# Kernel optimization log

Hardware: AMD Instinct MI355X
Metric: run time of the kernel (lower is better)

Reference implementation:

```python
import jax, jax.numpy as jnp
import numpy as np

B, N, D, RNN, K_TOPK = 32, 2000, 128, 640, 64


def setup_inputs() -> dict:
    key = jax.random.key(0)
    ks = jax.random.split(key, 16)
    s = 1.0 / np.sqrt(D)
    return {
        "Ahat": jax.random.uniform(ks[0], (B, N, N), dtype=jnp.float32),
        "node_embs": jax.random.normal(ks[1], (B, N, D), dtype=jnp.float32),
        "ht": jax.random.normal(ks[2], (B, RNN), dtype=jnp.float32),
        "prev_D": jax.random.normal(ks[3], (B, D, D), dtype=jnp.float32) * s,
        "mapper_w": jax.random.normal(ks[4], (D, RNN), dtype=jnp.float32) / np.sqrt(RNN),
        "mapper_b": jnp.zeros((D,), jnp.float32),
        "Wu": jax.random.normal(ks[5], (D, D), jnp.float32) * s,
        "Uu": jax.random.normal(ks[6], (D, D), jnp.float32) * s,
        "bu": jnp.zeros((D, D), jnp.float32),
        "Wr": jax.random.normal(ks[7], (D, D), jnp.float32) * s,
        "Ur": jax.random.normal(ks[8], (D, D), jnp.float32) * s,
        "br": jnp.zeros((D, D), jnp.float32),
        "Wh": jax.random.normal(ks[9], (D, D), jnp.float32) * s,
        "Uh": jax.random.normal(ks[10], (D, D), jnp.float32) * s,
        "bh": jnp.zeros((D, D), jnp.float32),
        "static_w": jax.random.normal(ks[11], (D, D), jnp.float32) * s,
    }


def _gate(W, U, b, x, h, act):
    # W,U: [D,D]; x,h: [B,D,D]; bias broadcasts over batch
    return act(jnp.einsum('ij,bjk->bik', W, x) + jnp.einsum('ij,bjk->bik', U, h) + b)


def reference(Ahat, node_embs, ht, prev_D, mapper_w, mapper_b,
              Wu, Uu, bu, Wr, Ur, br, Wh, Uh, bh, static_w):
    act = jax.nn.relu
    # ---- TopK_with_h ----
    scorer = jnp.tanh(jax.lax.stop_gradient(ht) @ mapper_w.T + mapper_b)     # [B,D]
    scores = jnp.einsum('bnd,bd->bn', node_embs, scorer)                      # [B,N]
    scores = scores / jnp.linalg.norm(scorer, axis=1, keepdims=True)
    _, topk_idx = jax.lax.top_k(scores, K_TOPK)                               # [B,K_TOPK]
    rep = D // K_TOPK + 1
    idx = jnp.tile(topk_idx, (1, rep))[:, :D]                                 # [B,D] selected node ids
    sel = jnp.take_along_axis(node_embs, idx[:, :, None], axis=1)             # [B,D,Dfeat]
    sel = sel * jnp.tanh(jnp.take_along_axis(scores, idx, axis=1))[..., None]
    logp = jax.nn.log_softmax(scores, axis=1)
    p = jnp.exp(logp)
    entropy = -(p * logp).sum(axis=1)                                         # [B]
    policy_score = jnp.take_along_axis(logp, idx, axis=1).mean(axis=1)        # [B]
    x = sel.transpose(0, 2, 1)                                                # [B,Dfeat,D]
    # ---- mat_GRU_cell: evolve GCN weights ----
    update = _gate(Wu, Uu, bu, x, prev_D, jax.nn.sigmoid)
    reset = _gate(Wr, Ur, br, x, prev_D, jax.nn.sigmoid)
    htilda = _gate(Wh, Uh, bh, x, reset * prev_D, jnp.tanh)
    Dw = (1.0 - update) * prev_D + update * htilda                            # [B,D,D]
    # ---- gather selected subgraph ----
    ne = jnp.take_along_axis(node_embs, idx[:, :, None], axis=1)              # [B,D,Dfeat]
    A = jnp.take_along_axis(Ahat, idx[:, :, None], axis=1)                    # [B,D,N]
    A = jnp.take_along_axis(A, idx[:, None, :], axis=2)                       # [B,D,D]
    di = A.sum(axis=1) ** -0.5                                                # [B,D]
    A = di[:, None, :] * A * jax.lax.stop_gradient(di[:, :, None])
    # ---- GCN with evolved + static weights ----
    h1 = act(jnp.einsum('bkj,bjd->bkd', A, jnp.einsum('bjd,bde->bje', ne, Dw)))
    h2 = act(jnp.einsum('bkj,bjd->bkd', A, jnp.einsum('bjd,de->bje', h1, static_w)))
    out = (h1 + h2) * 0.5                                                     # [B,D,Dfeat]
    return (out, policy_score, scorer, entropy)
```

## Files before the change

### kernel.cpp

```cpp
#include <hip/hip_runtime.h>
#include <math.h>


namespace {
constexpr int B_ = 32;
constexpr int N_ = 2000;
constexpr int D_ = 128;
constexpr int R_ = 640;

constexpr size_t OFF_SCORER = 0;
constexpr size_t OFF_INVN   = 4096;
constexpr size_t OFF_CANDV  = 4128;
constexpr size_t OFF_CANDI  = 20512;
constexpr size_t OFF_STATS  = 36896;
constexpr size_t OFF_TKI    = 37664;
constexpr size_t OFF_T0     = 39712;
constexpr size_t OFF_NE0T   = 41760;
constexpr size_t OFF_A0R    = 303904;
constexpr size_t OFF_DW     = 434976;
constexpr size_t OFF_H1     = 959264;

__global__ __launch_bounds__(1024) void k1_scorer(
    const float* __restrict__ ht, const float* __restrict__ mw,
    const float* __restrict__ mb, float* __restrict__ scorer,
    float* __restrict__ invn, float* __restrict__ outScorer) {
  const int b = blockIdx.x, t = threadIdx.x;
  const int d = t & 127, slice = t >> 7;
  __shared__ float sh[R_];
  __shared__ float part[8][128];
  __shared__ float red[2];
  for (int j = t; j < R_; j += 1024) sh[j] = ht[b * R_ + j];
  __syncthreads();
  const float* wp = mw + (size_t)d * R_ + slice * 80;
  const float* hh = sh + slice * 80;
  float acc = 0.f;
  #pragma unroll
  for (int j = 0; j < 80; j += 4) {
    float4 wv = *reinterpret_cast<const float4*>(wp + j);
    acc += wv.x * hh[j] + wv.y * hh[j + 1] + wv.z * hh[j + 2] + wv.w * hh[j + 3];
  }
  part[slice][d] = acc;
  __syncthreads();
  if (t < 128) {
    float a = mb[t];
    #pragma unroll
    for (int s = 0; s < 8; ++s) a += part[s][t];
    const float sv = tanhf(a);
    scorer[b * D_ + t] = sv;
    outScorer[b * D_ + t] = sv;
    float ss = sv * sv;
    #pragma unroll
    for (int o = 32; o > 0; o >>= 1) ss += __shfl_down(ss, o);
    if ((t & 63) == 0) red[t >> 6] = ss;
  }
  __syncthreads();
  if (t == 0) invn[b] = 1.0f / sqrtf(red[0] + red[1]);
}

__global__ __launch_bounds__(512) void k2_scores(
    const float* __restrict__ node, const float* __restrict__ scorer,
    const float* __restrict__ invn, float* __restrict__ cand_v,
    int* __restrict__ cand_i, float* __restrict__ stats) {
  const int b = blockIdx.x, c = blockIdx.y, t = threadIdx.x;
  const int cand = t & 255, s = t >> 8;
  const int lane = t & 63, w = t >> 6;
  __shared__ float sc[D_];
  __shared__ float pd[256][2];
  __shared__ float cv[256];
  __shared__ int ci[256];
  __shared__ int pr[256][2];
  __shared__ float r1[8], r2[8];
  if (t < D_) sc[t] = scorer[b * D_ + t];
  __syncthreads();
  const float inv = invn[b];
  const int n = c * 250 + cand;
  const bool valid = cand < 250;
  {
    float acc = 0.f;
    if (valid) {
      const float* row = node + ((size_t)b * N_ + n) * D_ + s * 64;
      const float* scp = sc + s * 64;
      #pragma unroll
      for (int j = 0; j < 64; j += 4) {
        float4 a = *reinterpret_cast<const float4*>(row + j);
        acc += a.x * scp[j] + a.y * scp[j + 1] + a.z * scp[j + 2] + a.w * scp[j + 3];
      }
    }
    pd[cand][s] = acc;
  }
  __syncthreads();
  float v = -INFINITY;
  if (s == 0 && valid) v = (pd[cand][0] + pd[cand][1]) * inv;
  float m = v;
  #pragma unroll
  for (int o = 32; o > 0; o >>= 1) m = fmaxf(m, __shfl_xor(m, o));
  if (lane == 0) r1[w] = m;
  __syncthreads();
  float Mc = r1[0];
  #pragma unroll
  for (int q = 1; q < 8; ++q) Mc = fmaxf(Mc, r1[q]);
  __syncthreads();
  float se = 0.f, sx = 0.f;
  if (s == 0 && valid) {
    const float x = v - Mc;
    const float e = expf(x);
    se = e;
    sx = x * e;
  }
  #pragma unroll
  for (int o = 32; o > 0; o >>= 1) {
    se += __shfl_xor(se, o);
    sx += __shfl_xor(sx, o);
  }
  if (lane == 0) { r1[w] = se; r2[w] = sx; }
  if (s == 0) {
    cv[cand] = v;
    ci[cand] = valid ? n : 0x7fffffff;
  }
  __syncthreads();
  if (t == 0) {
    float Se = 0.f, Sx = 0.f;
    #pragma unroll
    for (int q = 0; q < 8; ++q) { Se += r1[q]; Sx += r2[q]; }
    float* st = stats + ((size_t)b * 8 + c) * 3;
    st[0] = Mc;
    st[1] = Se;
    st[2] = Sx;
  }
  {
    const float mv = cv[cand];
    const int mi = ci[cand];
    int rank = 0;
    const int j0 = s * 128;
    for (int j = j0; j < j0 + 128; ++j) {
      const float jv = cv[j];
      const int ji = ci[j];
      rank += (jv > mv || (jv == mv && ji < mi)) ? 1 : 0;
    }
    pr[cand][s] = rank;
  }
  __syncthreads();
  if (s == 0 && valid) {
    const int rk = pr[cand][0] + pr[cand][1];
    if (rk < 64) {
      cand_v[((size_t)b * 8 + c) * 64 + rk] = cv[cand];
      cand_i[((size_t)b * 8 + c) * 64 + rk] = ci[cand];
    }
  }
}

__global__ __launch_bounds__(1024) void k3_merge(
    const float* __restrict__ cand_v, const int* __restrict__ cand_i,
    const float* __restrict__ stats, const float* __restrict__ node,
    const float* __restrict__ Ahat, int* __restrict__ tki,
    float* __restrict__ t0v, float* __restrict__ outPolicy,
    float* __restrict__ outEntropy, float* __restrict__ ne0T,
    float* __restrict__ A0r) {
  const int b = blockIdx.x, t = threadIdx.x;
  const int cand = t & 511, s = t >> 9;
  __shared__ float cv[512];
  __shared__ int ci[512];
  __shared__ int pr[512][2];
  __shared__ float sv[64];
  __shared__ int si[64];
  __shared__ float lne[64][132];
  if (t < 512) {
    cv[t] = cand_v[(size_t)b * 512 + t];
    ci[t] = cand_i[(size_t)b * 512 + t];
  }
  __syncthreads();
  {
    const float mv = cv[cand];
    const int mi = ci[cand];
    int rank = 0;
    const int j0 = s * 256;
    for (int j = j0; j < j0 + 256; ++j) {
      const float jv = cv[j];
      const int ji = ci[j];
      rank += (jv > mv || (jv == mv && ji < mi)) ? 1 : 0;
    }
    pr[cand][s] = rank;
  }
  __syncthreads();
  if (s == 0) {
    const int rk = pr[cand][0] + pr[cand][1];
    if (rk < 64) { sv[rk] = cv[cand]; si[rk] = ci[cand]; }
  }
  __syncthreads();
  {
    const float* Ab = Ahat + (size_t)b * N_ * N_;
    float* dst = A0r + (size_t)b * 4096;
    const int e0 = t * 4;
    #pragma unroll
    for (int j = 0; j < 4; ++j) {
      const int e = e0 + j;
      dst[e] = Ab[(size_t)si[e >> 6] * N_ + si[e & 63]];
    }
  }
  if (t < 64) {
    tki[b * 64 + t] = si[t];
    const float v = sv[t];
    t0v[b * 64 + t] = tanhf(v);
    float sum = v;
    #pragma unroll
    for (int o = 32; o > 0; o >>= 1) sum += __shfl_xor(sum, o);
    if (t == 0) {
      float M = -INFINITY;
      for (int c = 0; c < 8; ++c) M = fmaxf(M, stats[((size_t)b * 8 + c) * 3]);
      float se = 0.f, sx = 0.f;
      for (int c = 0; c < 8; ++c) {
        const float* st = stats + ((size_t)b * 8 + c) * 3;
        const float f = expf(st[0] - M);
        se += f * st[1];
        sx += f * (st[2] + (st[0] - M) * st[1]);
      }
      const float logS = logf(se);
      outPolicy[b] = sum * (1.0f / 64.0f) - M - logS;
      outEntropy[b] = logS - sx / se;
    }
  }
  __syncthreads();
  {
    const int k = t >> 4, q = t & 15;
    const float* src = node + ((size_t)b * N_ + si[k]) * D_ + q * 8;
    *reinterpret_cast<float4*>(&lne[k][q * 8]) =
        *reinterpret_cast<const float4*>(src);
    *reinterpret_cast<float4*>(&lne[k][q * 8 + 4]) =
        *reinterpret_cast<const float4*>(src + 4);
  }
  __syncthreads();
  {
    const int f = t >> 3, kh = (t & 7) * 8;
    float* dst = ne0T + ((size_t)b * D_ + f) * 64 + kh;
    float4 a, bq;
    a.x = lne[kh][f];     a.y = lne[kh + 1][f];
    a.z = lne[kh + 2][f]; a.w = lne[kh + 3][f];
    bq.x = lne[kh + 4][f]; bq.y = lne[kh + 5][f];
    bq.z = lne[kh + 6][f]; bq.w = lne[kh + 7][f];
    *reinterpret_cast<float4*>(dst) = a;
    *reinterpret_cast<float4*>(dst + 4) = bq;
  }
}

__global__ __launch_bounds__(256) void k5_gru(
    const float* __restrict__ Wu, const float* __restrict__ Uu, const float* __restrict__ bu,
    const float* __restrict__ Wr, const float* __restrict__ Ur, const float* __restrict__ br,
    const float* __restrict__ Wh, const float* __restrict__ Uh, const float* __restrict__ bh,
    const float* __restrict__ ne0T, const float* __restrict__ t0v,
    const float* __restrict__ P, float* __restrict__ Dw) {
  const int b = blockIdx.x, c = blockIdx.y;
  const int t = threadIdx.x;
  const int tx = t & 7, ty = t >> 3;
  const int sx_ = t & 15, sy_ = t >> 4;
  __shared__ float Wt[16][132], Ut[16][132];
  __shared__ float Xt[16][9], Yt[16][9];
  __shared__ float gs[2][128][9];
  __shared__ float t0s[8];
  const int col = c * 8 + tx;
  if (t < 8) t0s[t] = t0v[b * 64 + (c & 7) * 8 + t];
  const float* neT = ne0T + (size_t)b * D_ * 64;
  const float* Pb = P + (size_t)b * D_ * D_;
  for (int z = 0; z < 2; ++z) {
    const float* W = z ? Wr : Wu;
    const float* U = z ? Ur : Uu;
    const float* bb = z ? br : bu;
    float acc[4] = {};
    for (int f0 = 0; f0 < D_; f0 += 16) {
      __syncthreads();
      #pragma unroll
      for (int rr = 0; rr < 8; rr++) {
        const int i = rr * 16 + sy_;
        Wt[sx_][i] = W[i * D_ + f0 + sx_];
        Ut[sx_][i] = U[i * D_ + f0 + sx_];
      }
      if (t < 128) {
        const int ff = t >> 3, kk = t & 7;
        Xt[ff][kk] = neT[(f0 + ff) * 64 + (c & 7) * 8 + kk] * t0s[kk];
        Yt[ff][kk] = Pb[(f0 + ff) * D_ + c * 8 + kk];
      }
      __syncthreads();
      #pragma unroll
      for (int ff = 0; ff < 16; ff++) {
        const float xv = Xt[ff][tx];
        const float yv = Yt[ff][tx];
        const float4 wa = *reinterpret_cast<const float4*>(&Wt[ff][ty * 4]);
        const float4 ua = *reinterpret_cast<const float4*>(&Ut[ff][ty * 4]);
        acc[0] += wa.x * xv + ua.x * yv;
        acc[1] += wa.y * xv + ua.y * yv;
        acc[2] += wa.z * xv + ua.z * yv;
        acc[3] += wa.w * xv + ua.w * yv;
      }
    }
    #pragma unroll
    for (int r = 0; r < 4; r++) {
      const int i = ty * 4 + r;
      const float zz = acc[r] + bb[i * D_ + col];
      gs[z][i][tx] = 1.f / (1.f + expf(-zz));
    }
  }
  float acc[4] = {};
  for (int f0 = 0; f0 < D_; f0 += 16) {
    __syncthreads();
    #pragma unroll
    for (int rr = 0; rr < 8; rr++) {
      const int i = rr * 16 + sy_;
      Wt[sx_][i] = Wh[i * D_ + f0 + sx_];
      Ut[sx_][i] = Uh[i * D_ + f0 + sx_];
    }
    if (t < 128) {
      const int ff = t >> 3, kk = t & 7;
      Xt[ff][kk] = neT[(f0 + ff) * 64 + (c & 7) * 8 + kk] * t0s[kk];
      Yt[ff][kk] = gs[1][f0 + ff][kk] * Pb[(f0 + ff) * D_ + c * 8 + kk];
    }
    __syncthreads();
    #pragma unroll
    for (int ff = 0; ff < 16; ff++) {
      const float xv = Xt[ff][tx];
      const float yv = Yt[ff][tx];
      const float4 wa = *reinterpret_cast<const float4*>(&Wt[ff][ty * 4]);
      const float4 ua = *reinterpret_cast<const float4*>(&Ut[ff][ty * 4]);
      acc[0] += wa.x * xv + ua.x * yv;
      acc[1] += wa.y * xv + ua.y * yv;
      acc[2] += wa.z * xv + ua.z * yv;
      acc[3] += wa.w * xv + ua.w * yv;
    }
  }
  #pragma unroll
  for (int r = 0; r < 4; r++) {
    const int i = ty * 4 + r;
    const size_t off = ((size_t)b * D_ + i) * D_ + col;
    const float hh = tanhf(acc[r] + bh[i * D_ + col]);
    const float uu = gs[0][i][tx];
    const float pp = Pb[i * D_ + col];
    Dw[off] = (1.f - uu) * pp + uu * hh;
  }
}

__global__ __launch_bounds__(256) void k6_gcn1(
    const float* __restrict__ ne0T, const float* __restrict__ Dw,
    const float* __restrict__ A0r, float* __restrict__ h1ws) {
  const int b = blockIdx.x, c = blockIdx.y;
  const int t = threadIdx.x;
  const int tx = t & 15, ty = t >> 4;
  const int colg = t & 3, rowg = t >> 2;
  __shared__ float As[64][68];
  __shared__ float di[64];
  __shared__ float At[16][68];
  __shared__ float Bt[16][20];
  __shared__ float Ts[64][20];
  const float* Ab = A0r + (size_t)b * 4096;
  const float* neT = ne0T + (size_t)b * D_ * 64;
  const float* Db = Dw + (size_t)b * D_ * D_;
  #pragma unroll
  for (int ph = 0; ph < 4; ++ph) {
    const int i = ph * 16 + ty;
    *reinterpret_cast<float4*>(&As[i][tx * 4]) =
        *reinterpret_cast<const float4*>(Ab + i * 64 + tx * 4);
  }
  __syncthreads();
  if (t < 64) {
    float s = 0.f;
    #pragma unroll
    for (int i = 0; i < 64; ++i) s += As[i][t];
    di[t] = 1.0f / sqrtf(2.0f * s);
  }
  __syncthreads();
  #pragma unroll
  for (int ph = 0; ph < 4; ++ph) {
    const int i = ph * 16 + ty;
    const float sI = 2.0f * di[i];
    float4 v = *reinterpret_cast<float4*>(&As[i][tx * 4]);
    v.x *= sI * di[tx * 4];
    v.y *= sI * di[tx * 4 + 1];
    v.z *= sI * di[tx * 4 + 2];
    v.w *= sI * di[tx * 4 + 3];
    *reinterpret_cast<float4*>(&As[i][tx * 4]) = v;
  }
  float acc[4] = {};
  for (int f0 = 0; f0 < D_; f0 += 16) {
    __syncthreads();
    {
      *reinterpret_cast<float4*>(&At[ty][tx * 4]) =
          *reinterpret_cast<const float4*>(neT + (f0 + ty) * 64 + tx * 4);
      Bt[ty][tx] = Db[(f0 + ty) * D_ + c * 16 + tx];
    }
    __syncthreads();
    #pragma unroll
    for (int ff = 0; ff < 16; ff++) {
      const float a = At[ff][rowg];
      const float4 b4 = *reinterpret_cast<const float4*>(&Bt[ff][colg * 4]);
      acc[0] += a * b4.x;
      acc[1] += a * b4.y;
      acc[2] += a * b4.z;
      acc[3] += a * b4.w;
    }
  }
  __syncthreads();
  {
    float4 o = {acc[0], acc[1], acc[2], acc[3]};
    *reinterpret_cast<float4*>(&Ts[rowg][colg * 4]) = o;
  }
  __syncthreads();
  float acc2[4] = {};
  for (int ff = 0; ff < 64; ++ff) {
    const float a = As[rowg][ff];
    const float4 b4 = *reinterpret_cast<const float4*>(&Ts[ff][colg * 4]);
    acc2[0] += a * b4.x;
    acc2[1] += a * b4.y;
    acc2[2] += a * b4.z;
    acc2[3] += a * b4.w;
  }
  {
    float4 o = {fmaxf(acc2[0], 0.f), fmaxf(acc2[1], 0.f),
                fmaxf(acc2[2], 0.f), fmaxf(acc2[3], 0.f)};
    *reinterpret_cast<float4*>(h1ws + ((size_t)b * 64 + rowg) * D_ +
                               c * 16 + colg * 4) = o;
  }
}

__global__ __launch_bounds__(256) void k7_gcn2(
    const float* __restrict__ h1ws, const float* __restrict__ sw,
    const float* __restrict__ A0r, float* __restrict__ out) {
  const int b = blockIdx.x, c = blockIdx.y;
  const int t = threadIdx.x;
  const int tx = t & 15, ty = t >> 4;
  const int colg = t & 3, rowg = t >> 2;
  __shared__ float As[64][68];
  __shared__ float di[64];
  __shared__ float At[16][68];
  __shared__ float Bt[16][20];
  __shared__ float Ts[64][20];
  const float* Ab = A0r + (size_t)b * 4096;
  const float* h1b = h1ws + (size_t)b * 64 * D_;
  #pragma unroll
  for (int ph = 0; ph < 4; ++ph) {
    const int i = ph * 16 + ty;
    *reinterpret_cast<float4*>(&As[i][tx * 4]) =
        *reinterpret_cast<const float4*>(Ab + i * 64 + tx * 4);
  }
  __syncthreads();
  if (t < 64) {
    float s = 0.f;
    #pragma unroll
    for (int i = 0; i < 64; ++i) s += As[i][t];
    di[t] = 1.0f / sqrtf(2.0f * s);
  }
  __syncthreads();
  #pragma unroll
  for (int ph = 0; ph < 4; ++ph) {
    const int i = ph * 16 + ty;
    const float sI = 2.0f * di[i];
    float4 v = *reinterpret_cast<float4*>(&As[i][tx * 4]);
    v.x *= sI * di[tx * 4];
    v.y *= sI * di[tx * 4 + 1];
    v.z *= sI * di[tx * 4 + 2];
    v.w *= sI * di[tx * 4 + 3];
    *reinterpret_cast<float4*>(&As[i][tx * 4]) = v;
  }
  float acc[4] = {};
  for (int f0 = 0; f0 < D_; f0 += 16) {
    __syncthreads();
    {
      const int i4 = tx * 4;
      #pragma unroll
      for (int s = 0; s < 4; ++s)
        At[ty][i4 + s] = h1b[(i4 + s) * D_ + f0 + ty];
      Bt[ty][tx] = sw[(f0 + ty) * D_ + c * 16 + tx];
    }
    __syncthreads();
    #pragma unroll
    for (int ff = 0; ff < 16; ff++) {
      const float a = At[ff][rowg];
      const float4 b4 = *reinterpret_cast<const float4*>(&Bt[ff][colg * 4]);
      acc[0] += a * b4.x;
      acc[1] += a * b4.y;
      acc[2] += a * b4.z;
      acc[3] += a * b4.w;
    }
  }
  __syncthreads();
  {
    float4 o = {acc[0], acc[1], acc[2], acc[3]};
    *reinterpret_cast<float4*>(&Ts[rowg][colg * 4]) = o;
  }
  __syncthreads();
  float acc2[4] = {};
  for (int ff = 0; ff < 64; ++ff) {
    const float a = As[rowg][ff];
    const float4 b4 = *reinterpret_cast<const float4*>(&Ts[ff][colg * 4]);
    acc2[0] += a * b4.x;
    acc2[1] += a * b4.y;
    acc2[2] += a * b4.z;
    acc2[3] += a * b4.w;
  }
  {
    const int k = c * 16 + colg * 4;
    const float4 h1v = *reinterpret_cast<const float4*>(h1b + rowg * D_ + k);
    float4 o;
    o.x = 0.5f * (h1v.x + fmaxf(acc2[0], 0.f));
    o.y = 0.5f * (h1v.y + fmaxf(acc2[1], 0.f));
    o.z = 0.5f * (h1v.z + fmaxf(acc2[2], 0.f));
    o.w = 0.5f * (h1v.w + fmaxf(acc2[3], 0.f));
    *reinterpret_cast<float4*>(out + ((size_t)b * D_ + rowg) * D_ + k) = o;
    *reinterpret_cast<float4*>(out + ((size_t)b * D_ + rowg + 64) * D_ + k) = o;
  }
}

}

extern "C" void kernel_launch(void* const* d_in, const int* in_sizes, int n_in,
                              void* d_out, int out_size, void* d_ws, size_t ws_size,
                              hipStream_t stream) {
  (void)in_sizes; (void)n_in; (void)out_size; (void)ws_size;
  const float* Ahat = (const float*)d_in[0];
  const float* node = (const float*)d_in[1];
  const float* ht   = (const float*)d_in[2];
  const float* prevD= (const float*)d_in[3];
  const float* mw   = (const float*)d_in[4];
  const float* mb   = (const float*)d_in[5];
  const float* Wu   = (const float*)d_in[6];
  const float* Uu   = (const float*)d_in[7];
  const float* bu   = (const float*)d_in[8];
  const float* Wr   = (const float*)d_in[9];
  const float* Ur   = (const float*)d_in[10];
  const float* br   = (const float*)d_in[11];
  const float* Wh   = (const float*)d_in[12];
  const float* Uh   = (const float*)d_in[13];
  const float* bh   = (const float*)d_in[14];
  const float* sw   = (const float*)d_in[15];

  float* out = (float*)d_out;
  float* outPolicy  = out + (size_t)B_ * D_ * D_;
  float* outScorer  = outPolicy + B_;
  float* outEntropy = outScorer + (size_t)B_ * D_;

  float* ws = (float*)d_ws;
  float* scorer = ws + OFF_SCORER;
  float* invn   = ws + OFF_INVN;
  float* cand_v = ws + OFF_CANDV;
  int*   cand_i = (int*)(ws + OFF_CANDI);
  float* stats  = ws + OFF_STATS;
  int*   tki    = (int*)(ws + OFF_TKI);
  float* t0v    = ws + OFF_T0;
  float* ne0T   = ws + OFF_NE0T;
  float* A0r    = ws + OFF_A0R;
  float* Dw     = ws + OFF_DW;
  float* h1ws   = ws + OFF_H1;

  k1_scorer<<<B_, 1024, 0, stream>>>(ht, mw, mb, scorer, invn, outScorer);
  k2_scores<<<dim3(B_, 8), 512, 0, stream>>>(node, scorer, invn, cand_v, cand_i, stats);
  k3_merge<<<B_, 1024, 0, stream>>>(cand_v, cand_i, stats, node, Ahat, tki, t0v,
                                    outPolicy, outEntropy, ne0T, A0r);
  k5_gru<<<dim3(B_, 16), 256, 0, stream>>>(Wu, Uu, bu, Wr, Ur, br, Wh, Uh, bh,
                                           ne0T, t0v, prevD, Dw);
  k6_gcn1<<<dim3(B_, 8), 256, 0, stream>>>(ne0T, Dw, A0r, h1ws);
  k7_gcn2<<<dim3(B_, 8), 256, 0, stream>>>(h1ws, sw, A0r, out);
}
```

Baseline: 123.1 us.

## Give each wavefront private smem tiles and replace block barriers with wave barriers

The GRU and both GCN kernels are restructured so that each 64-lane wavefront stages its own slice of the weight and activation tiles in private shared memory. Block-wide __syncthreads in the inner K loops become wave barriers. The GRU kernel also fuses the update and reset gate passes into one loop that shares the X/Y tiles, and uses vectorized float4 global loads. The aim is to cut barrier stalls and redundant tile loads, at the cost of more shared memory per block and some duplicated X/Y staging across waves.

```diff
diff --git a/kernel.cpp b/kernel.cpp
--- a/kernel.cpp
+++ b/kernel.cpp
@@ -250,89 +250,122 @@
     const float* __restrict__ P, float* __restrict__ Dw) {
   const int b = blockIdx.x, c = blockIdx.y;
   const int t = threadIdx.x;
-  const int tx = t & 7, ty = t >> 3;
-  const int sx_ = t & 15, sy_ = t >> 4;
-  __shared__ float Wt[16][132], Ut[16][132];
-  __shared__ float Xt[16][9], Yt[16][9];
-  __shared__ float gs[2][128][9];
-  __shared__ float t0s[8];
+  const int w = t >> 6, l = t & 63;
+  const int tx = l & 7, ry = l >> 3;
+  __shared__ float WA[4][16][40], UA[4][16][40];
+  __shared__ float WB[4][16][40], UB[4][16][40];
+  __shared__ float Xl[4][16][8], Yl[4][16][8];
+  __shared__ float gr[128][9];
+  const int row0 = w * 32;
   const int col = c * 8 + tx;
-  if (t < 8) t0s[t] = t0v[b * 64 + (c & 7) * 8 + t];
+  const float t0c = t0v[b * 64 + (c & 7) * 8 + tx];
   const float* neT = ne0T + (size_t)b * D_ * 64;
   const float* Pb = P + (size_t)b * D_ * D_;
-  for (int z = 0; z < 2; ++z) {
-    const float* W = z ? Wr : Wu;
-    const float* U = z ? Ur : Uu;
-    const float* bb = z ? br : bu;
-    float acc[4] = {};
-    for (int f0 = 0; f0 < D_; f0 += 16) {
-      __syncthreads();
+  const int sr = l >> 1, h = l & 1;
+  const int e0 = l * 2;
+  const int xff = e0 >> 3, xkk = e0 & 7;
+
+  float aU[4] = {}, aR[4] = {};
+  for (int f0 = 0; f0 < D_; f0 += 16) {
+    {
+      const size_t rb = (size_t)(row0 + sr) * D_ + f0 + h * 8;
+      const float4 wu0 = *reinterpret_cast<const float4*>(Wu + rb);
+      const float4 wu1 = *reinterpret_cast<const float4*>(Wu + rb + 4);
+      const float4 uu0 = *reinterpret_cast<const float4*>(Uu + rb);
+      const float4 uu1 = *reinterpret_cast<const float4*>(Uu + rb + 4);
+      const float4 wr0 = *reinterpret_cast<const float4*>(Wr + rb);
+      const float4 wr1 = *reinterpret_cast<const float4*>(Wr + rb + 4);
+      const float4 ur0 = *reinterpret_cast<const float4*>(Ur + rb);
+      const float4 ur1 = *reinterpret_cast<const float4*>(Ur + rb + 4);
+      const float wuv[8] = {wu0.x, wu0.y, wu0.z, wu0.w, wu1.x, wu1.y, wu1.z, wu1.w};
+      const float uuv[8] = {uu0.x, uu0.y, uu0.z, uu0.w, uu1.x, uu1.y, uu1.z, uu1.w};
+      const float wrv[8] = {wr0.x, wr0.y, wr0.z, wr0.w, wr1.x, wr1.y, wr1.z, wr1.w};
+      const float urv[8] = {ur0.x, ur0.y, ur0.z, ur0.w, ur1.x, ur1.y, ur1.z, ur1.w};
       #pragma unroll
-      for (int rr = 0; rr < 8; rr++) {
-        const int i = rr * 16 + sy_;
-        Wt[sx_][i] = W[i * D_ + f0 + sx_];
-        Ut[sx_][i] = U[i * D_ + f0 + sx_];
+      for (int j = 0; j < 8; ++j) {
+        WA[w][h * 8 + j][sr] = wuv[j];
+        UA[w][h * 8 + j][sr] = uuv[j];
+        WB[w][h * 8 + j][sr] = wrv[j];
+        UB[w][h * 8 + j][sr] = urv[j];
       }
-      if (t < 128) {
-        const int ff = t >> 3, kk = t & 7;
-        Xt[ff][kk] = neT[(f0 + ff) * 64 + (c & 7) * 8 + kk] * t0s[kk];
-        Yt[ff][kk] = Pb[(f0 + ff) * D_ + c * 8 + kk];
+      #pragma unroll
+      for (int e = 0; e < 2; ++e) {
+        const int ff = xff, kk = xkk + e;
+        Xl[w][ff][kk] = neT[(f0 + ff) * 64 + (c & 7) * 8 + kk];
+        Yl[w][ff][kk] = Pb[(size_t)(f0 + ff) * D_ + c * 8 + kk];
       }
-      __syncthreads();
+    }
+    __builtin_amdgcn_wave_barrier();
+    #pragma unroll
+    for (int ff = 0; ff < 16; ++ff) {
+      const float xv = Xl[w][ff][tx] * t0c;
+      const float yv = Yl[w][ff][tx];
+      const float4 wa = *reinterpret_cast<const float4*>(&WA[w][ff][ry * 4]);
+      const float4 ua = *reinterpret_cast<const float4*>(&UA[w][ff][ry * 4]);
+      const float4 wb = *reinterpret_cast<const float4*>(&WB[w][ff][ry * 4]);
+      const float4 ub = *reinterpret_cast<const float4*>(&UB[w][ff][ry * 4]);
+      aU[0] += wa.x * xv + ua.x * yv;
+      aU[1] += wa.y * xv + ua.y * yv;
+      aU[2] += wa.z * xv + ua.z * yv;
+      aU[3] += wa.w * xv + ua.w * yv;
+      aR[0] += wb.x * xv + ub.x * yv;
+      aR[1] += wb.y * xv + ub.y * yv;
+      aR[2] += wb.z * xv + ub.z * yv;
+      aR[3] += wb.w * xv + ub.w * yv;
+    }
+    __builtin_amdgcn_wave_barrier();
+  }
+  float uval[4];
+  #pragma unroll
+  for (int r = 0; r < 4; ++r) {
+    const int i = row0 + ry * 4 + r;
+    uval[r] = 1.f / (1.f + expf(-(aU[r] + bu[i * D_ + col])));
+    gr[i][tx] = 1.f / (1.f + expf(-(aR[r] + br[i * D_ + col])));
+  }
+  __syncthreads();
+
+  float aH[4] = {};
+  for (int f0 = 0; f0 < D_; f0 += 16) {
+    {
+      const size_t rb = (size_t)(row0 + sr) * D_ + f0 + h * 8;
+      const float4 wh0 = *reinterpret_cast<const float4*>(Wh + rb);
+      const float4 wh1 = *reinterpret_cast<const float4*>(Wh + rb + 4);
+      const float4 uh0 = *reinterpret_cast<const float4*>(Uh + rb);
+      const float4 uh1 = *reinterpret_cast<const float4*>(Uh + rb + 4);
+      const float whv[8] = {wh0.x, wh0.y, wh0.z, wh0.w, wh1.x, wh1.y, wh1.z, wh1.w};
+      const float uhv[8] = {uh0.x, uh0.y, uh0.z, uh0.w, uh1.x, uh1.y, uh1.z, uh1.w};
       #pragma unroll
-      for (int ff = 0; ff < 16; ff++) {
-        const float xv = Xt[ff][tx];
-        const float yv = Yt[ff][tx];
-        const float4 wa = *reinterpret_cast<const float4*>(&Wt[ff][ty * 4]);
-        const float4 ua = *reinterpret_cast<const float4*>(&Ut[ff][ty * 4]);
-        acc[0] += wa.x * xv + ua.x * yv;
-        acc[1] += wa.y * xv + ua.y * yv;
-        acc[2] += wa.z * xv + ua.z * yv;
-        acc[3] += wa.w * xv + ua.w * yv;
+      for (int j = 0; j < 8; ++j) {
+        WA[w][h * 8 + j][sr] = whv[j];
+        UA[w][h * 8 + j][sr] = uhv[j];
       }
-    }
-    #pragma unroll
-    for (int r = 0; r < 4; r++) {
-      const int i = ty * 4 + r;
-      const float zz = acc[r] + bb[i * D_ + col];
-      gs[z][i][tx] = 1.f / (1.f + expf(-zz));
-    }
-  }
-  float acc[4] = {};
-  for (int f0 = 0; f0 < D_; f0 += 16) {
-    __syncthreads();
-    #pragma unroll
-    for (int rr = 0; rr < 8; rr++) {
-      const int i = rr * 16 + sy_;
-      Wt[sx_][i] = Wh[i * D_ + f0 + sx_];
-      Ut[sx_][i] = Uh[i * D_ + f0 + sx_];
-    }
-    if (t < 128) {
-      const int ff = t >> 3, kk = t & 7;
-      Xt[ff][kk] = neT[(f0 + ff) * 64 + (c & 7) * 8 + kk] * t0s[kk];
-      Yt[ff][kk] = gs[1][f0 + ff][kk] * Pb[(f0 + ff) * D_ + c * 8 + kk];
-    }
-    __syncthreads();
-    #pragma unroll
-    for (int ff = 0; ff < 16; ff++) {
-      const float xv = Xt[ff][tx];
-      const float yv = Yt[ff][tx];
-      const float4 wa = *reinterpret_cast<const float4*>(&Wt[ff][ty * 4]);
-      const float4 ua = *reinterpret_cast<const float4*>(&Ut[ff][ty * 4]);
-      acc[0] += wa.x * xv + ua.x * yv;
-      acc[1] += wa.y * xv + ua.y * yv;
-      acc[2] += wa.z * xv + ua.z * yv;
-      acc[3] += wa.w * xv + ua.w * yv;
-    }
-  }
-  #pragma unroll
-  for (int r = 0; r < 4; r++) {
-    const int i = ty * 4 + r;
-    const size_t off = ((size_t)b * D_ + i) * D_ + col;
-    const float hh = tanhf(acc[r] + bh[i * D_ + col]);
-    const float uu = gs[0][i][tx];
-    const float pp = Pb[i * D_ + col];
-    Dw[off] = (1.f - uu) * pp + uu * hh;
+      #pragma unroll
+      for (int e = 0; e < 2; ++e) {
+        const int ff = xff, kk = xkk + e;
+        Xl[w][ff][kk] = neT[(f0 + ff) * 64 + (c & 7) * 8 + kk];
+        Yl[w][ff][kk] = gr[f0 + ff][kk] * Pb[(size_t)(f0 + ff) * D_ + c * 8 + kk];
+      }
+    }
+    __builtin_amdgcn_wave_barrier();
+    #pragma unroll
+    for (int ff = 0; ff < 16; ++ff) {
+      const float xv = Xl[w][ff][tx] * t0c;
+      const float yv = Yl[w][ff][tx];
+      const float4 wa = *reinterpret_cast<const float4*>(&WA[w][ff][ry * 4]);
+      const float4 ua = *reinterpret_cast<const float4*>(&UA[w][ff][ry * 4]);
+      aH[0] += wa.x * xv + ua.x * yv;
+      aH[1] += wa.y * xv + ua.y * yv;
+      aH[2] += wa.z * xv + ua.z * yv;
+      aH[3] += wa.w * xv + ua.w * yv;
+    }
+    __builtin_amdgcn_wave_barrier();
+  }
+  #pragma unroll
+  for (int r = 0; r < 4; ++r) {
+    const int i = row0 + ry * 4 + r;
+    const float hh = tanhf(aH[r] + bh[i * D_ + col]);
+    const float pp = Pb[(size_t)i * D_ + col];
+    Dw[((size_t)b * D_ + i) * D_ + col] = (1.f - uval[r]) * pp + uval[r] * hh;
   }
 }
 
@@ -341,13 +374,14 @@
     const float* __restrict__ A0r, float* __restrict__ h1ws) {
   const int b = blockIdx.x, c = blockIdx.y;
   const int t = threadIdx.x;
+  const int w = t >> 6, l = t & 63;
   const int tx = t & 15, ty = t >> 4;
-  const int colg = t & 3, rowg = t >> 2;
+  const int cg = l & 3, rg = l >> 2;
+  const int row = w * 16 + rg;
   __shared__ float As[64][68];
   __shared__ float di[64];
-  __shared__ float At[16][68];
-  __shared__ float Bt[16][20];
-  __shared__ float Ts[64][20];
+  __shared__ float Ts[64][24];
+  __shared__ float At[4][16][24], Bt[4][16][24];
   const float* Ab = A0r + (size_t)b * 4096;
   const float* neT = ne0T + (size_t)b * D_ * 64;
   const float* Db = Dw + (size_t)b * D_ * D_;
@@ -376,45 +410,45 @@
     v.w *= sI * di[tx * 4 + 3];
     *reinterpret_cast<float4*>(&As[i][tx * 4]) = v;
   }
+  const int sff = l >> 2, sq = (l & 3) * 4;
   float acc[4] = {};
   for (int f0 = 0; f0 < D_; f0 += 16) {
-    __syncthreads();
     {
-      *reinterpret_cast<float4*>(&At[ty][tx * 4]) =
-          *reinterpret_cast<const float4*>(neT + (f0 + ty) * 64 + tx * 4);
-      Bt[ty][tx] = Db[(f0 + ty) * D_ + c * 16 + tx];
-    }
-    __syncthreads();
-    #pragma unroll
-    for (int ff = 0; ff < 16; ff++) {
-      const float a = At[ff][rowg];
-      const float4 b4 = *reinterpret_cast<const float4*>(&Bt[ff][colg * 4]);
+      const float4 av = *reinterpret_cast<const float4*>(neT + (f0 + sff) * 64 + w * 16 + sq);
+      *reinterpret_cast<float4*>(&At[w][sff][sq]) = av;
+      const float4 bv = *reinterpret_cast<const float4*>(Db + (size_t)(f0 + sff) * D_ + c * 16 + sq);
+      *reinterpret_cast<float4*>(&Bt[w][sff][sq]) = bv;
+    }
+    __builtin_amdgcn_wave_barrier();
+    #pragma unroll
+    for (int ff = 0; ff < 16; ++ff) {
+      const float a = At[w][ff][rg];
+      const float4 b4 = *reinterpret_cast<const float4*>(&Bt[w][ff][cg * 4]);
       acc[0] += a * b4.x;
       acc[1] += a * b4.y;
       acc[2] += a * b4.z;
       acc[3] += a * b4.w;
     }
-  }
-  __syncthreads();
+    __builtin_amdgcn_wave_barrier();
+  }
   {
     float4 o = {acc[0], acc[1], acc[2], acc[3]};
-    *reinterpret_cast<float4*>(&Ts[rowg][colg * 4]) = o;
-  }
-  __syncthreads();
-  float acc2[4] = {};
+    *reinterpret_cast<float4*>(&Ts[row][cg * 4]) = o;
+  }
+  __syncthreads();
+  float a2[4] = {};
   for (int ff = 0; ff < 64; ++ff) {
-    const float a = As[rowg][ff];
-    const float4 b4 = *reinterpret_cast<const float4*>(&Ts[ff][colg * 4]);
-    acc2[0] += a * b4.x;
-    acc2[1] += a * b4.y;
-    acc2[2] += a * b4.z;
-    acc2[3] += a * b4.w;
-  }
-  {
-    float4 o = {fmaxf(acc2[0], 0.f), fmaxf(acc2[1], 0.f),
-                fmaxf(acc2[2], 0.f), fmaxf(acc2[3], 0.f)};
-    *reinterpret_cast<float4*>(h1ws + ((size_t)b * 64 + rowg) * D_ +
-                               c * 16 + colg * 4) = o;
+    const float a = As[row][ff];
+    const float4 b4 = *reinterpret_cast<const float4*>(&Ts[ff][cg * 4]);
+    a2[0] += a * b4.x;
+    a2[1] += a * b4.y;
+    a2[2] += a * b4.z;
+    a2[3] += a * b4.w;
+  }
+  {
+    float4 o = {fmaxf(a2[0], 0.f), fmaxf(a2[1], 0.f),
+                fmaxf(a2[2], 0.f), fmaxf(a2[3], 0.f)};
+    *reinterpret_cast<float4*>(h1ws + ((size_t)b * 64 + row) * D_ + c * 16 + cg * 4) = o;
   }
 }
 
@@ -423,13 +457,14 @@
     const float* __restrict__ A0r, float* __restrict__ out) {
   const int b = blockIdx.x, c = blockIdx.y;
   const int t = threadIdx.x;
+  const int w = t >> 6, l = t & 63;
   const int tx = t & 15, ty = t >> 4;
-  const int colg = t & 3, rowg = t >> 2;
+  const int cg = l & 3, rg = l >> 2;
+  const int row = w * 16 + rg;
   __shared__ float As[64][68];
   __shared__ float di[64];
-  __shared__ float At[16][68];
-  __shared__ float Bt[16][20];
-  __shared__ float Ts[64][20];
+  __shared__ float Ts[64][24];
+  __shared__ float At[4][16][24], Bt[4][16][24];
   const float* Ab = A0r + (size_t)b * 4096;
   const float* h1b = h1ws + (size_t)b * 64 * D_;
   #pragma unroll
@@ -457,52 +492,56 @@
     v.w *= sI * di[tx * 4 + 3];
     *reinterpret_cast<float4*>(&As[i][tx * 4]) = v;
   }
+  const int sr16 = l & 15, sh4 = l >> 4;
+  const int sff = l >> 2, sq = (l & 3) * 4;
   float acc[4] = {};
   for (int f0 = 0; f0 < D_; f0 += 16) {
-    __syncthreads();
     {
-      const int i4 = tx * 4;
-      #pragma unroll
-      for (int s = 0; s < 4; ++s)
-        At[ty][i4 + s] = h1b[(i4 + s) * D_ + f0 + ty];
-      Bt[ty][tx] = sw[(f0 + ty) * D_ + c * 16 + tx];
-    }
-    __syncthreads();
-    #pragma unroll
-    for (int ff = 0; ff < 16; ff++) {
-      const float a = At[ff][rowg];
-      const float4 b4 = *reinterpret_cast<const float4*>(&Bt[ff][colg * 4]);
+      const float4 hv = *reinterpret_cast<const float4*>(
+          h1b + (size_t)(w * 16 + sr16) * D_ + f0 + sh4 * 4);
+      At[w][sh4 * 4 + 0][sr16] = hv.x;
+      At[w][sh4 * 4 + 1][sr16] = hv.y;
+      At[w][sh4 * 4 + 2][sr16] = hv.z;
+      At[w][sh4 * 4 + 3][sr16] = hv.w;
+      const float4 bv = *reinterpret_cast<const float4*>(sw + (size_t)(f0 + sff) * D_ + c * 16 + sq);
+      *reinterpret_cast<float4*>(&Bt[w][sff][sq]) = bv;
+    }
+    __builtin_amdgcn_wave_barrier();
+    #pragma unroll
+    for (int ff = 0; ff < 16; ++ff) {
+      const float a = At[w][ff][rg];
+      const float4 b4 = *reinterpret_cast<const float4*>(&Bt[w][ff][cg * 4]);
       acc[0] += a * b4.x;
       acc[1] += a * b4.y;
       acc[2] += a * b4.z;
       acc[3] += a * b4.w;
     }
-  }
-  __syncthreads();
+    __builtin_amdgcn_wave_barrier();
+  }
   {
     float4 o = {acc[0], acc[1], acc[2], acc[3]};
-    *reinterpret_cast<float4*>(&Ts[rowg][colg * 4]) = o;
-  }
-  __syncthreads();
-  float acc2[4] = {};
+    *reinterpret_cast<float4*>(&Ts[row][cg * 4]) = o;
+  }
+  __syncthreads();
+  float a2[4] = {};
   for (int ff = 0; ff < 64; ++ff) {
-    const float a = As[rowg][ff];
-    const float4 b4 = *reinterpret_cast<const float4*>(&Ts[ff][colg * 4]);
-    acc2[0] += a * b4.x;
-    acc2[1] += a * b4.y;
-    acc2[2] += a * b4.z;
-    acc2[3] += a * b4.w;
-  }
-  {
-    const int k = c * 16 + colg * 4;
-    const float4 h1v = *reinterpret_cast<const float4*>(h1b + rowg * D_ + k);
+    const float a = As[row][ff];
+    const float4 b4 = *reinterpret_cast<const float4*>(&Ts[ff][cg * 4]);
+    a2[0] += a * b4.x;
+    a2[1] += a * b4.y;
+    a2[2] += a * b4.z;
+    a2[3] += a * b4.w;
+  }
+  {
+    const int k = c * 16 + cg * 4;
+    const float4 h1v = *reinterpret_cast<const float4*>(h1b + (size_t)row * D_ + k);
     float4 o;
-    o.x = 0.5f * (h1v.x + fmaxf(acc2[0], 0.f));
-    o.y = 0.5f * (h1v.y + fmaxf(acc2[1], 0.f));
-    o.z = 0.5f * (h1v.z + fmaxf(acc2[2], 0.f));
-    o.w = 0.5f * (h1v.w + fmaxf(acc2[3], 0.f));
-    *reinterpret_cast<float4*>(out + ((size_t)b * D_ + rowg) * D_ + k) = o;
-    *reinterpret_cast<float4*>(out + ((size_t)b * D_ + rowg + 64) * D_ + k) = o;
+    o.x = 0.5f * (h1v.x + fmaxf(a2[0], 0.f));
+    o.y = 0.5f * (h1v.y + fmaxf(a2[1], 0.f));
+    o.z = 0.5f * (h1v.z + fmaxf(a2[2], 0.f));
+    o.w = 0.5f * (h1v.w + fmaxf(a2[3], 0.f));
+    *reinterpret_cast<float4*>(out + ((size_t)b * D_ + row) * D_ + k) = o;
+    *reinterpret_cast<float4*>(out + ((size_t)b * D_ + row + 64) * D_ + k) = o;
   }
 }
 
```

Result: faster. 117.8 us (median of 2 runs) (-4.3%).
